# Kernel optimization log

Hardware: AMD Instinct MI355X
Metric: run time of the kernel (lower is better)

The kernel has to match this reference:

```python
import jax, jax.numpy as jnp
from jax import lax
import numpy as np

EPS = 1e-5
COMMITMENT = 0.25


def conv1d(x, w, b, pad):
    # x: [N,C,T], w: [O,I,K]
    y = lax.conv_general_dilated(x, w, window_strides=(1,), padding=[(pad, pad)],
                                 dimension_numbers=('NCH', 'OIH', 'NCH'))
    return y + b[None, :, None]


def batchnorm(x, g, b):
    # training-mode BN (PyTorch default): batch stats over (N, T), biased var
    m = jnp.mean(x, axis=(0, 2), keepdims=True)
    v = jnp.var(x, axis=(0, 2), keepdims=True)
    return (x - m) * lax.rsqrt(v + EPS) * g[None, :, None] + b[None, :, None]


def setup_inputs() -> dict:
    key = jax.random.key(0)
    ks = jax.random.split(key, 16)
    B, C_in, T = 16, 80, 4096
    H1, H2, D, K = 128, 256, 64, 512
    s = 0.05
    inp = {
        'x': jax.random.normal(ks[0], (B, C_in, T), jnp.float32),
        # encoder
        'enc_w1': jax.random.normal(ks[1], (H1, C_in, 3), jnp.float32) * s,
        'enc_b1': jnp.zeros((H1,), jnp.float32),
        'bn1_g': jnp.ones((H1,), jnp.float32), 'bn1_b': jnp.zeros((H1,), jnp.float32),
        'enc_w2': jax.random.normal(ks[2], (H2, H1, 3), jnp.float32) * s,
        'enc_b2': jnp.zeros((H2,), jnp.float32),
        'bn2_g': jnp.ones((H2,), jnp.float32), 'bn2_b': jnp.zeros((H2,), jnp.float32),
        'enc_w3': jax.random.normal(ks[3], (D, H2, 1), jnp.float32) * s,
        'enc_b3': jnp.zeros((D,), jnp.float32),
        # codebook, init uniform(-1/K, 1/K) like the torch module
        'codebook': jax.random.uniform(ks[4], (K, D), jnp.float32, -1.0 / K, 1.0 / K),
        # decoder (hidden_dims reversed: [256, 128])
        'dec_w1': jax.random.normal(ks[5], (H2, D, 3), jnp.float32) * s,
        'dec_b1': jnp.zeros((H2,), jnp.float32),
        'dbn1_g': jnp.ones((H2,), jnp.float32), 'dbn1_b': jnp.zeros((H2,), jnp.float32),
        'dec_w2': jax.random.normal(ks[6], (H1, H2, 3), jnp.float32) * s,
        'dec_b2': jnp.zeros((H1,), jnp.float32),
        'dbn2_g': jnp.ones((H1,), jnp.float32), 'dbn2_b': jnp.zeros((H1,), jnp.float32),
        'dec_w3': jax.random.normal(ks[7], (C_in, H1, 3), jnp.float32) * s,
        'dec_b3': jnp.zeros((C_in,), jnp.float32),
    }
    return inp


def _vqvae(x, enc_w1, enc_b1, bn1_g, bn1_b, enc_w2, enc_b2, bn2_g, bn2_b,
           enc_w3, enc_b3, codebook, dec_w1, dec_b1, dbn1_g, dbn1_b,
           dec_w2, dec_b2, dbn2_g, dbn2_b, dec_w3, dec_b3):
    # ---- Encoder ----
    h = jax.nn.relu(batchnorm(conv1d(x, enc_w1, enc_b1, 1), bn1_g, bn1_b))
    h = jax.nn.relu(batchnorm(conv1d(h, enc_w2, enc_b2, 1), bn2_g, bn2_b))
    z = conv1d(h, enc_w3, enc_b3, 0)  # [B, D, T]

    # ---- Vector Quantizer ----
    B, D, T = z.shape
    zt = jnp.transpose(z, (0, 2, 1))            # [B, T, D]
    flat = zt.reshape(-1, D)                    # [B*T, D]
    # squared L2 distances to codebook [B*T, K]
    d2 = (jnp.sum(flat * flat, axis=1, keepdims=True)
          + jnp.sum(codebook * codebook, axis=1)
          - 2.0 * flat @ codebook.T)
    idx = jnp.argmin(d2, axis=1)                # [B*T]
    quantized = codebook[idx].reshape(B, T, D)  # gather == onehot @ codebook

    e_latent_loss = jnp.mean((lax.stop_gradient(quantized) - zt) ** 2)
    q_latent_loss = jnp.mean((quantized - lax.stop_gradient(zt)) ** 2)
    vq_loss = q_latent_loss + COMMITMENT * e_latent_loss

    # straight-through estimator
    q_st = zt + lax.stop_gradient(quantized - zt)
    q_st = jnp.transpose(q_st, (0, 2, 1))       # [B, D, T]
    encoding_indices = idx.reshape(B, T)

    # ---- Decoder ----
    h = conv1d(q_st, dec_w1, dec_b1, 1)
    h = conv1d(jax.nn.relu(batchnorm(h, dbn1_g, dbn1_b)), dec_w2, dec_b2, 1)
    recon = conv1d(jax.nn.relu(batchnorm(h, dbn2_g, dbn2_b)), dec_w3, dec_b3, 1)
    return recon, vq_loss, encoding_indices


def reference(x, enc_w1, enc_b1, bn1_g, bn1_b, enc_w2, enc_b2, bn2_g, bn2_b,
              enc_w3, enc_b3, codebook, dec_w1, dec_b1, dbn1_g, dbn1_b,
              dec_w2, dec_b2, dbn2_g, dbn2_b, dec_w3, dec_b3):
    return _vqvae(x, enc_w1, enc_b1, bn1_g, bn1_b, enc_w2, enc_b2, bn2_g, bn2_b,
                  enc_w3, enc_b3, codebook, dec_w1, dec_b1, dbn1_g, dbn1_b,
                  dec_w2, dec_b2, dbn2_g, dbn2_b, dec_w3, dec_b3)
```

## Files before the change

### kernel.cpp

```cpp
#include <hip/hip_runtime.h>
#include <math.h>

#define N_B 16
#define T_LEN 4096

typedef float f32x4  __attribute__((ext_vector_type(4)));
typedef _Float16 half8 __attribute__((ext_vector_type(8)));

static const size_t OFF_A    = 0;
static const size_t OFF_B    = 8388608;
static const size_t OFF_Z    = 25165824;
static const size_t OFF_WS   = 29360128;
static const size_t OFF_CBS  = 29540352;
static const size_t OFF_C2   = 29683712;
static const size_t OFF_ST   = 29684736;
static const size_t OFF_LOSS = 29685760;

static const size_t WS_E1 = 0;
static const size_t WS_E2 = 36864;
static const size_t WS_E3 = 135168;
static const size_t WS_D1 = 0;
static const size_t WS_D2 = 49152;
static const size_t WS_D3 = 147456;

__device__ inline void f2h2(float v, short& hi, short& lo) {
    _Float16 h = (_Float16)v;
    float r = (v - (float)h) * 4096.0f;
    _Float16 l = (_Float16)r;
    hi = __builtin_bit_cast(short, h);
    lo = __builtin_bit_cast(short, l);
}

template<int C_IN, int C_OUT, int KS>
__device__ inline void wsplit_fill(const float* __restrict__ w,
                                   short* __restrict__ dst, int e) {
    int i  = e & 31;
    int r  = e >> 5;
    int co = r % C_OUT;
    int r2 = r / C_OUT;
    int k  = r2 % KS;
    int c  = r2 / KS;
    int ci = c * 32 + i;
    float v = (ci < C_IN) ? w[((size_t)co * C_IN + ci) * KS + k] : 0.f;
    short h, l; f2h2(v, h, l);
    size_t base = ((size_t)(c * KS + k) * 2 * C_OUT + co) * 32 + i;
    dst[base] = h;
    dst[base + (size_t)C_OUT * 32] = l;
}

__global__ __launch_bounds__(256) void prep_k(
        const float* __restrict__ w1, const float* __restrict__ w2,
        const float* __restrict__ w3, const float* __restrict__ cb,
        float* wsf) {
    int e = blockIdx.x * 256 + threadIdx.x;
    if (e < 36864)        wsplit_fill<80, 128, 3>(w1, (short*)(wsf + OFF_WS + WS_E1), e);
    else if (e < 135168)  wsplit_fill<128, 256, 3>(w2, (short*)(wsf + OFF_WS + WS_E2), e - 36864);
    else if (e < 151552)  wsplit_fill<256, 64, 1>(w3, (short*)(wsf + OFF_WS + WS_E3), e - 135168);
    else if (e < 152064) {
        int c = e - 151552;
        const float* p = cb + (size_t)c * 64;
        double s = 0.0;
        for (int d = 0; d < 64; ++d) { double v = p[d]; s += v * v; }
        wsf[OFF_C2 + c] = (float)s;
    } else if (e < 184832) {
        int e2   = e - 152064;
        int i    = e2 & 31;
        int r    = e2 >> 5;
        int code = r & 511;
        int ks   = r >> 9;
        float v  = cb[(size_t)code * 64 + ks * 32 + i];
        short h, l; f2h2(v, h, l);
        short* dst = (short*)(wsf + OFF_CBS);
        dst[((size_t)(ks * 2 + 0) * 512 + code) * 32 + i] = h;
        dst[((size_t)(ks * 2 + 1) * 512 + code) * 32 + i] = l;
    } else if (e == 184832) {
        *(double*)(wsf + OFF_LOSS) = 0.0;
    }
}

__global__ __launch_bounds__(256) void prep2_k(
        const float* __restrict__ wd1, const float* __restrict__ wd2,
        const float* __restrict__ wd3, float* wsf) {
    int e = blockIdx.x * 256 + threadIdx.x;
    if (e < 49152)        wsplit_fill<64, 256, 3>(wd1, (short*)(wsf + OFF_WS + WS_D1), e);
    else if (e < 147456)  wsplit_fill<256, 128, 3>(wd2, (short*)(wsf + OFF_WS + WS_D2), e - 49152);
    else if (e < 178176)  wsplit_fill<128, 80, 3>(wd3, (short*)(wsf + OFF_WS + WS_D3), e - 147456);
}

template<int C_IN, int C_OUT, int KS, bool BN_IN>
__global__ __launch_bounds__(256, 3) void fconv_k(
        const float* __restrict__ x, const short* __restrict__ wsp,
        const float* __restrict__ bias, const float2* __restrict__ stats,
        float* __restrict__ out) {
    constexpr int NCH  = (C_IN + 31) / 32;
    constexpr int HALO = KS / 2;
    constexpr int TT   = (KS == 1) ? 64 : 128;
    constexpr int NTT  = TT / 16;
    constexpr int NTILE = T_LEN / TT;
    constexpr int XR   = TT + KS - 1;
    constexpr int RS   = 72;
    constexpr int LO   = 40;
    constexpr int TQ   = TT / 4;

    __shared__ __align__(16) short xs[XR * RS];

    const int tid  = threadIdx.x;
    const int lane = tid & 63;
    const int wv   = tid >> 6;
    const int ln   = lane & 15;
    const int q    = lane >> 4;

    const int n    = blockIdx.x / NTILE;
    const int t0   = (blockIdx.x % NTILE) * TT;
    const int co0  = blockIdx.y * 64;
    const int co_l = co0 + wv * 16 + ln;

    f32x4 a0[NTT], a1[NTT];
#pragma unroll
    for (int tt = 0; tt < NTT; ++tt)
#pragma unroll
        for (int i = 0; i < 4; ++i) { a0[tt][i] = 0.f; a1[tt][i] = 0.f; }

#pragma unroll 1
    for (int c = 0; c < NCH; ++c) {
        half8 ah[KS], al[KS];
        {
            half8 z = {0, 0, 0, 0, 0, 0, 0, 0};
#pragma unroll
            for (int k = 0; k < KS; ++k) {
                const short* wp = wsp
                    + ((size_t)(c * KS + k) * 2 * C_OUT + co_l) * 32 + q * 8;
                ah[k] = (co_l < C_OUT) ? *(const half8*)wp : z;
                al[k] = (co_l < C_OUT) ? *(const half8*)(wp + (size_t)C_OUT * 32) : z;
            }
        }

        __syncthreads();
        for (int e = tid; e < 32 * TQ; e += 256) {
            const int ci  = e / TQ;
            const int tq  = e % TQ;
            const int cig = c * 32 + ci;
            float v[4] = {0.f, 0.f, 0.f, 0.f};
            if (cig < C_IN) {
                const float* xp = x + ((size_t)(n * C_IN + cig)) * T_LEN + t0 + tq;
#pragma unroll
                for (int j = 0; j < 4; ++j) v[j] = xp[TQ * j];
                if constexpr (BN_IN) {
                    float2 s = stats[cig];
#pragma unroll
                    for (int j = 0; j < 4; ++j) v[j] = fmaxf(fmaf(v[j], s.x, s.y), 0.f);
                }
            }
#pragma unroll
            for (int j = 0; j < 4; ++j) {
                short h, l; f2h2(v[j], h, l);
                short* p = &xs[(HALO + tq + TQ * j) * RS + ci];
                p[0]  = h;
                p[LO] = l;
            }
        }
        if constexpr (KS == 3) {
            if (tid < 64) {
                const int ci   = tid & 31;
                const int side = tid >> 5;
                const int cig  = c * 32 + ci;
                const int gt   = side ? (t0 + TT) : (t0 - 1);
                float v = 0.f;
                if (cig < C_IN && gt >= 0 && gt < T_LEN) {
                    v = x[((size_t)(n * C_IN + cig)) * T_LEN + gt];
                    if constexpr (BN_IN) {
                        float2 s = stats[cig];
                        v = fmaxf(fmaf(v, s.x, s.y), 0.f);
                    }
                }
                short h, l; f2h2(v, h, l);
                short* p = &xs[(side ? (XR - 1) : 0) * RS + ci];
                p[0] = h; p[LO] = l;
            }
        }
        __syncthreads();

#pragma unroll
        for (int k = 0; k < KS; ++k) {
#pragma unroll
            for (int tt = 0; tt < NTT; ++tt) {
                const short* xr = &xs[(tt * 16 + ln + k) * RS + q * 8];
                half8 bh = *(const half8*)&xr[0];
                half8 bl = *(const half8*)&xr[LO];
                a0[tt] = __builtin_amdgcn_mfma_f32_16x16x32_f16(ah[k], bh, a0[tt], 0, 0, 0);
                a1[tt] = __builtin_amdgcn_mfma_f32_16x16x32_f16(ah[k], bl, a1[tt], 0, 0, 0);
                a1[tt] = __builtin_amdgcn_mfma_f32_16x16x32_f16(al[k], bh, a1[tt], 0, 0, 0);
            }
        }
    }

#pragma unroll
    for (int r = 0; r < 4; ++r) {
        const int co = co0 + wv * 16 + q * 4 + r;
        if (co < C_OUT) {
            const float bv = bias[co];
            float* op = out + ((size_t)(n * C_OUT + co)) * T_LEN + t0 + ln;
#pragma unroll
            for (int tt = 0; tt < NTT; ++tt)
                op[tt * 16] = fmaf(a1[tt][r], 0.000244140625f, a0[tt][r]) + bv;
        }
    }
}

__global__ __launch_bounds__(256) void stats1_k(
        const float* __restrict__ y, int C, double2* __restrict__ part) {
    int c = blockIdx.x % C, n = blockIdx.x / C;
    int tid = threadIdx.x;
    const float* p = y + ((size_t)(n * C + c)) * T_LEN;
    double s1 = 0.0, s2 = 0.0;
    for (int t = tid; t < T_LEN; t += 256) {
        double v = p[t];
        s1 += v; s2 += v * v;
    }
    __shared__ double r1[256], r2[256];
    r1[tid] = s1; r2[tid] = s2;
    __syncthreads();
    for (int s = 128; s > 0; s >>= 1) {
        if (tid < s) { r1[tid] += r1[tid + s]; r2[tid] += r2[tid + s]; }
        __syncthreads();
    }
    if (tid == 0) part[(size_t)c * N_B + n] = make_double2(r1[0], r2[0]);
}

__global__ __launch_bounds__(256) void stats2_k(
        const double2* __restrict__ part, int C, const float* __restrict__ g,
        const float* __restrict__ b, float2* __restrict__ stats) {
    int c = blockIdx.x * 256 + threadIdx.x;
    if (c >= C) return;
    double s1 = 0.0, s2 = 0.0;
    for (int n = 0; n < N_B; ++n) {
        double2 v = part[(size_t)c * N_B + n];
        s1 += v.x; s2 += v.y;
    }
    double m   = s1 / 65536.0;
    double var = s2 / 65536.0 - m * m;
    double sc  = (double)g[c] / sqrt(var + 1e-5);
    stats[c] = make_float2((float)sc, (float)((double)b[c] - m * sc));
}

__global__ __launch_bounds__(256) void vq_k(
        const float* __restrict__ z, const float* __restrict__ cb,
        const short* __restrict__ cbs, const float* __restrict__ c2,
        float* __restrict__ q, float* __restrict__ idx_out,
        double* __restrict__ loss) {
    __shared__ __align__(16) float zs[64 * 68];
    __shared__ __align__(16) short zh[64 * 136];
    __shared__ float  c2s[512];
    __shared__ float  szf_s[64];
    __shared__ int    idxs[64];
    __shared__ double dred[256];

    const int tid  = threadIdx.x;
    const int lane = tid & 63;
    const int wv   = tid >> 6;
    const int ln   = lane & 15;
    const int q4   = lane >> 4;
    const int n    = blockIdx.x >> 6;
    const int t0   = (blockIdx.x & 63) * 64;

    for (int e = tid; e < 512; e += 256) c2s[e] = c2[e];
    for (int e = tid; e < 1024; e += 256) {
        const int d  = e >> 4;
        const int tq = e & 15;
        const float* zp = z + ((size_t)(n * 64 + d)) * T_LEN + t0 + tq;
        const int ks = d >> 5, i = d & 31;
#pragma unroll
        for (int j = 0; j < 4; ++j) {
            const int t = tq + 16 * j;
            float v = zp[16 * j];
            zs[t * 68 + d] = v;
            short h, l; f2h2(v, h, l);
            zh[t * 136 + (ks * 2 + 0) * 32 + i] = h;
            zh[t * 136 + (ks * 2 + 1) * 32 + i] = l;
        }
    }
    __syncthreads();
    if (tid < 64) {
        double s = 0.0;
        const float* zr = &zs[tid * 68];
        for (int d = 0; d < 64; ++d) { double v = zr[d]; s += v * v; }
        szf_s[tid] = (float)s;
    }
    __syncthreads();

    const short* zr = &zh[(wv * 16 + ln) * 136 + q4 * 8];
    const half8 bh0 = *(const half8*)&zr[0];
    const half8 bl0 = *(const half8*)&zr[32];
    const half8 bh1 = *(const half8*)&zr[64];
    const half8 bl1 = *(const half8*)&zr[96];
    const float As  = szf_s[wv * 16 + ln];

    float bs = 3.0e38f;
    int   bi = 1 << 30;

#pragma unroll 4
    for (int ct = 0; ct < 32; ++ct) {
        const short* ap = cbs + ((size_t)(ct * 16 + ln)) * 32 + q4 * 8;
        const half8 ah0 = *(const half8*)&ap[0];
        const half8 al0 = *(const half8*)&ap[512 * 32];
        const half8 ah1 = *(const half8*)&ap[2 * 512 * 32];
        const half8 al1 = *(const half8*)&ap[3 * 512 * 32];
        f32x4 a0 = {0.f, 0.f, 0.f, 0.f};
        f32x4 a1 = {0.f, 0.f, 0.f, 0.f};
        a0 = __builtin_amdgcn_mfma_f32_16x16x32_f16(ah0, bh0, a0, 0, 0, 0);
        a1 = __builtin_amdgcn_mfma_f32_16x16x32_f16(ah0, bl0, a1, 0, 0, 0);
        a1 = __builtin_amdgcn_mfma_f32_16x16x32_f16(al0, bh0, a1, 0, 0, 0);
        a0 = __builtin_amdgcn_mfma_f32_16x16x32_f16(ah1, bh1, a0, 0, 0, 0);
        a1 = __builtin_amdgcn_mfma_f32_16x16x32_f16(ah1, bl1, a1, 0, 0, 0);
        a1 = __builtin_amdgcn_mfma_f32_16x16x32_f16(al1, bh1, a1, 0, 0, 0);
#pragma unroll
        for (int r = 0; r < 4; ++r) {
            const int code = ct * 16 + q4 * 4 + r;
            const float m32 = fmaf(a1[r], 0.000244140625f, a0[r]);
            const float A   = As + c2s[code];
            const float s   = A - 2.0f * m32;
            if (s < bs || (s == bs && code < bi)) { bs = s; bi = code; }
        }
    }
#pragma unroll
    for (int off = 16; off <= 32; off <<= 1) {
        const float os = __shfl_xor(bs, off);
        const int   oi = __shfl_xor(bi, off);
        if (os < bs || (os == bs && oi < bi)) { bs = os; bi = oi; }
    }
    if (q4 == 0) {
        const int t = wv * 16 + ln;
        idxs[t] = bi;
        idx_out[(size_t)n * T_LEN + t0 + t] = (float)bi;
    }
    __syncthreads();

    {
        const int g = tid >> 6, t = tid & 63;
        const int bi2 = idxs[t];
        double ls = 0.0;
        for (int dd = 0; dd < 16; ++dd) {
            const int d = g * 16 + dd;
            const float qv = cb[(size_t)bi2 * 64 + d];
            const float zv = zs[t * 68 + d];
            const double df = (double)qv - (double)zv;
            ls += df * df;
            q[((size_t)(n * 64 + d)) * T_LEN + t0 + t] = qv;
        }
        dred[tid] = ls;
    }
    __syncthreads();
    for (int s = 128; s > 0; s >>= 1) {
        if (tid < s) dred[tid] += dred[tid + s];
        __syncthreads();
    }
    if (tid == 0) atomicAdd(loss, dred[0]);
}

__global__ void fin_k(const double* __restrict__ loss, float* __restrict__ out) {
    if (threadIdx.x == 0 && blockIdx.x == 0)
        out[0] = (float)(1.25 * (*loss) / 4194304.0);
}

extern "C" void kernel_launch(void* const* d_in, const int* in_sizes, int n_in,
                              void* d_out, int out_size, void* d_ws, size_t ws_size,
                              hipStream_t stream) {
    const float* x      = (const float*)d_in[0];
    const float* enc_w1 = (const float*)d_in[1];
    const float* enc_b1 = (const float*)d_in[2];
    const float* bn1_g  = (const float*)d_in[3];
    const float* bn1_b  = (const float*)d_in[4];
    const float* enc_w2 = (const float*)d_in[5];
    const float* enc_b2 = (const float*)d_in[6];
    const float* bn2_g  = (const float*)d_in[7];
    const float* bn2_b  = (const float*)d_in[8];
    const float* enc_w3 = (const float*)d_in[9];
    const float* enc_b3 = (const float*)d_in[10];
    const float* cb     = (const float*)d_in[11];
    const float* dec_w1 = (const float*)d_in[12];
    const float* dec_b1 = (const float*)d_in[13];
    const float* dbn1_g = (const float*)d_in[14];
    const float* dbn1_b = (const float*)d_in[15];
    const float* dec_w2 = (const float*)d_in[16];
    const float* dec_b2 = (const float*)d_in[17];
    const float* dbn2_g = (const float*)d_in[18];
    const float* dbn2_b = (const float*)d_in[19];
    const float* dec_w3 = (const float*)d_in[20];
    const float* dec_b3 = (const float*)d_in[21];

    float* wsf   = (float*)d_ws;
    float* outf  = (float*)d_out;
    float* A     = wsf + OFF_A;
    float* Bb    = wsf + OFF_B;
    float* Z     = wsf + OFF_Z;
    float2* st   = (float2*)(wsf + OFF_ST);
    double* lossp = (double*)(wsf + OFF_LOSS);
    double2* partA = (double2*)A;
    double2* partB = (double2*)Bb;

    const short* wsE1 = (const short*)(wsf + OFF_WS + WS_E1);
    const short* wsE2 = (const short*)(wsf + OFF_WS + WS_E2);
    const short* wsE3 = (const short*)(wsf + OFF_WS + WS_E3);
    const short* wsD1 = (const short*)(wsf + OFF_WS + WS_D1);
    const short* wsD2 = (const short*)(wsf + OFF_WS + WS_D2);
    const short* wsD3 = (const short*)(wsf + OFF_WS + WS_D3);
    const short* cbs  = (const short*)(wsf + OFF_CBS);

    prep_k<<<723, 256, 0, stream>>>(enc_w1, enc_w2, enc_w3, cb, wsf);

    fconv_k<80, 128, 3, false><<<dim3(512, 2), 256, 0, stream>>>(
        x, wsE1, enc_b1, nullptr, A);
    stats1_k<<<128 * N_B, 256, 0, stream>>>(A, 128, partB);
    stats2_k<<<1, 256, 0, stream>>>(partB, 128, bn1_g, bn1_b, st);
    fconv_k<128, 256, 3, true><<<dim3(512, 4), 256, 0, stream>>>(
        A, wsE2, enc_b2, st, Bb);
    stats1_k<<<256 * N_B, 256, 0, stream>>>(Bb, 256, partA);
    stats2_k<<<1, 256, 0, stream>>>(partA, 256, bn2_g, bn2_b, st);
    fconv_k<256, 64, 1, true><<<dim3(1024, 1), 256, 0, stream>>>(
        Bb, wsE3, enc_b3, st, Z);

    prep2_k<<<696, 256, 0, stream>>>(dec_w1, dec_w2, dec_w3, wsf);

    vq_k<<<1024, 256, 0, stream>>>(Z, cb, cbs, wsf + OFF_C2, Z,
                                   outf + 5242881, lossp);
    fin_k<<<1, 64, 0, stream>>>(lossp, outf + 5242880);

    fconv_k<64, 256, 3, false><<<dim3(512, 4), 256, 0, stream>>>(
        Z, wsD1, dec_b1, nullptr, Bb);
    stats1_k<<<256 * N_B, 256, 0, stream>>>(Bb, 256, partA);
    stats2_k<<<1, 256, 0, stream>>>(partA, 256, dbn1_g, dbn1_b, st);
    fconv_k<256, 128, 3, true><<<dim3(512, 2), 256, 0, stream>>>(
        Bb, wsD2, dec_b2, st, A);
    stats1_k<<<128 * N_B, 256, 0, stream>>>(A, 128, partB);
    stats2_k<<<1, 256, 0, stream>>>(partB, 128, dbn2_g, dbn2_b, st);
    fconv_k<128, 80, 3, true><<<dim3(512, 2), 256, 0, stream>>>(
        A, wsD3, dec_b3, st, outf);
}
```

Before: 412.4 us.

## Switch convs to 32x32 MFMA tiles and fuse BN stats into conv epilogue

The conv kernel moves from 16x16x32 MFMA to 32x32x16 MFMA with a 2x2 wave layout and separate hi/lo LDS planes, and the split weights are repacked in 16-channel groups. Each conv epilogue now produces per-block double sums and sum-of-squares, so the separate stats1/stats2 passes that re-read the full activation are replaced by a single small reduction kernel. A runtime self-test of the MFMA layout is added with a scalar FMA fallback path. The occupancy hint drops from 3 to 2 blocks per SM to accommodate the larger accumulators.

Measured after the change: 553.4 us. 34.2% more time.

```diff
diff --git a/kernel.cpp b/kernel.cpp
--- a/kernel.cpp
+++ b/kernel.cpp
@@ -5,7 +5,10 @@
 #define T_LEN 4096
 
 typedef float f32x4  __attribute__((ext_vector_type(4)));
+typedef float f32x16 __attribute__((ext_vector_type(16)));
 typedef _Float16 half8 __attribute__((ext_vector_type(8)));
+
+struct LL { long a, b; };
 
 static const size_t OFF_A    = 0;
 static const size_t OFF_B    = 8388608;
@@ -30,22 +33,25 @@
     hi = __builtin_bit_cast(short, h);
     lo = __builtin_bit_cast(short, l);
 }
+__device__ inline float h2f(short s) {
+    return (float)__builtin_bit_cast(_Float16, s);
+}
 
 template<int C_IN, int C_OUT, int KS>
 __device__ inline void wsplit_fill(const float* __restrict__ w,
                                    short* __restrict__ dst, int e) {
-    int i  = e & 31;
-    int r  = e >> 5;
+    int i  = e & 15;
+    int r  = e >> 4;
     int co = r % C_OUT;
     int r2 = r / C_OUT;
     int k  = r2 % KS;
-    int c  = r2 / KS;
-    int ci = c * 32 + i;
+    int c2 = r2 / KS;
+    int ci = c2 * 16 + i;
     float v = (ci < C_IN) ? w[((size_t)co * C_IN + ci) * KS + k] : 0.f;
     short h, l; f2h2(v, h, l);
-    size_t base = ((size_t)(c * KS + k) * 2 * C_OUT + co) * 32 + i;
+    size_t base = ((size_t)(c2 * KS + k) * 2 * C_OUT + co) * 16 + i;
     dst[base] = h;
-    dst[base + (size_t)C_OUT * 32] = l;
+    dst[base + (size_t)C_OUT * 16] = l;
 }
 
 __global__ __launch_bounds__(256) void prep_k(
@@ -87,54 +93,72 @@
     else if (e < 178176)  wsplit_fill<128, 80, 3>(wd3, (short*)(wsf + OFF_WS + WS_D3), e - 147456);
 }
 
-template<int C_IN, int C_OUT, int KS, bool BN_IN>
-__global__ __launch_bounds__(256, 3) void fconv_k(
+template<int C_IN, int C_OUT, int KS, bool BN_IN, bool STATS>
+__global__ __launch_bounds__(256, 2) void fconv_k(
         const float* __restrict__ x, const short* __restrict__ wsp,
         const float* __restrict__ bias, const float2* __restrict__ stats,
-        float* __restrict__ out) {
-    constexpr int NCH  = (C_IN + 31) / 32;
-    constexpr int HALO = KS / 2;
-    constexpr int TT   = (KS == 1) ? 64 : 128;
-    constexpr int NTT  = TT / 16;
+        float* __restrict__ out, double2* __restrict__ part) {
+    constexpr int NCH   = (C_IN + 31) / 32;
+    constexpr int HALO  = KS / 2;
+    constexpr int TT    = (KS == 1) ? 64 : 128;
+    constexpr int HT    = TT / 2;
+    constexpr int NTT   = HT / 32;
     constexpr int NTILE = T_LEN / TT;
-    constexpr int XR   = TT + KS - 1;
-    constexpr int RS   = 72;
-    constexpr int LO   = 40;
-    constexpr int TQ   = TT / 4;
-
-    __shared__ __align__(16) short xs[XR * RS];
+    constexpr int XR    = TT + KS - 1;
+    constexpr int RS2   = 36;
+    constexpr int TQ    = TT / 4;
+
+    __shared__ __align__(16) short xh[XR * RS2];
+    __shared__ __align__(16) short xl[XR * RS2];
+    __shared__ int okf;
 
     const int tid  = threadIdx.x;
     const int lane = tid & 63;
     const int wv   = tid >> 6;
-    const int ln   = lane & 15;
-    const int q    = lane >> 4;
+    const int wr   = wv >> 1;
+    const int wc   = wv & 1;
+    const int nn   = lane & 31;
+    const int hsel = lane >> 5;
 
     const int n    = blockIdx.x / NTILE;
     const int t0   = (blockIdx.x % NTILE) * TT;
     const int co0  = blockIdx.y * 64;
-    const int co_l = co0 + wv * 16 + ln;
-
-    f32x4 a0[NTT], a1[NTT];
+    const int co_l = co0 + wr * 32 + nn;
+
+    bool ok = true;
+    {
+        half8 pa, pb;
+#pragma unroll
+        for (int j = 0; j < 8; ++j) {
+            int k = hsel * 8 + j;
+            pa[j] = (_Float16)(float)(nn + 2 * k);
+            pb[j] = (_Float16)(float)(nn + 3 * k);
+        }
+        f32x16 pd;
+#pragma unroll
+        for (int r = 0; r < 16; ++r) pd[r] = 0.f;
+        pd = __builtin_amdgcn_mfma_f32_32x32x16_f16(pa, pb, pd, 0, 0, 0);
+#pragma unroll
+        for (int r = 0; r < 16; ++r) {
+            int m = (r & 3) + 8 * (r >> 2) + 4 * hsel;
+            float e = (float)(16 * m * nn + 360 * m + 240 * nn + 7440);
+            if (pd[r] != e) ok = false;
+        }
+    }
+    if (tid == 0) okf = 1;
+    __syncthreads();
+    if (!ok) okf = 0;
+    __syncthreads();
+    const bool okp = (okf != 0);
+
+    f32x16 a0[NTT], a1[NTT];
 #pragma unroll
     for (int tt = 0; tt < NTT; ++tt)
 #pragma unroll
-        for (int i = 0; i < 4; ++i) { a0[tt][i] = 0.f; a1[tt][i] = 0.f; }
+        for (int r = 0; r < 16; ++r) { a0[tt][r] = 0.f; a1[tt][r] = 0.f; }
 
 #pragma unroll 1
     for (int c = 0; c < NCH; ++c) {
-        half8 ah[KS], al[KS];
-        {
-            half8 z = {0, 0, 0, 0, 0, 0, 0, 0};
-#pragma unroll
-            for (int k = 0; k < KS; ++k) {
-                const short* wp = wsp
-                    + ((size_t)(c * KS + k) * 2 * C_OUT + co_l) * 32 + q * 8;
-                ah[k] = (co_l < C_OUT) ? *(const half8*)wp : z;
-                al[k] = (co_l < C_OUT) ? *(const half8*)(wp + (size_t)C_OUT * 32) : z;
-            }
-        }
-
         __syncthreads();
         for (int e = tid; e < 32 * TQ; e += 256) {
             const int ci  = e / TQ;
@@ -145,77 +169,147 @@
                 const float* xp = x + ((size_t)(n * C_IN + cig)) * T_LEN + t0 + tq;
 #pragma unroll
                 for (int j = 0; j < 4; ++j) v[j] = xp[TQ * j];
-                if constexpr (BN_IN) {
-                    float2 s = stats[cig];
-#pragma unroll
-                    for (int j = 0; j < 4; ++j) v[j] = fmaxf(fmaf(v[j], s.x, s.y), 0.f);
+                if (BN_IN) {
+                    float2 sst = stats[cig];
+#pragma unroll
+                    for (int j = 0; j < 4; ++j) v[j] = fmaxf(fmaf(v[j], sst.x, sst.y), 0.f);
                 }
             }
 #pragma unroll
             for (int j = 0; j < 4; ++j) {
                 short h, l; f2h2(v[j], h, l);
-                short* p = &xs[(HALO + tq + TQ * j) * RS + ci];
-                p[0]  = h;
-                p[LO] = l;
+                const int row = HALO + tq + TQ * j;
+                xh[row * RS2 + ci] = h;
+                xl[row * RS2 + ci] = l;
             }
         }
-        if constexpr (KS == 3) {
+        if (KS == 3) {
             if (tid < 64) {
                 const int ci   = tid & 31;
                 const int side = tid >> 5;
                 const int cig  = c * 32 + ci;
                 const int gt   = side ? (t0 + TT) : (t0 - 1);
-                float v = 0.f;
+                float vv = 0.f;
                 if (cig < C_IN && gt >= 0 && gt < T_LEN) {
-                    v = x[((size_t)(n * C_IN + cig)) * T_LEN + gt];
-                    if constexpr (BN_IN) {
-                        float2 s = stats[cig];
-                        v = fmaxf(fmaf(v, s.x, s.y), 0.f);
+                    vv = x[((size_t)(n * C_IN + cig)) * T_LEN + gt];
+                    if (BN_IN) {
+                        float2 sst = stats[cig];
+                        vv = fmaxf(fmaf(vv, sst.x, sst.y), 0.f);
                     }
                 }
-                short h, l; f2h2(v, h, l);
-                short* p = &xs[(side ? (XR - 1) : 0) * RS + ci];
-                p[0] = h; p[LO] = l;
+                short h, l; f2h2(vv, h, l);
+                const int row = side ? (XR - 1) : 0;
+                xh[row * RS2 + ci] = h;
+                xl[row * RS2 + ci] = l;
             }
         }
         __syncthreads();
 
-#pragma unroll
-        for (int k = 0; k < KS; ++k) {
-#pragma unroll
-            for (int tt = 0; tt < NTT; ++tt) {
-                const short* xr = &xs[(tt * 16 + ln + k) * RS + q * 8];
-                half8 bh = *(const half8*)&xr[0];
-                half8 bl = *(const half8*)&xr[LO];
-                a0[tt] = __builtin_amdgcn_mfma_f32_16x16x32_f16(ah[k], bh, a0[tt], 0, 0, 0);
-                a1[tt] = __builtin_amdgcn_mfma_f32_16x16x32_f16(ah[k], bl, a1[tt], 0, 0, 0);
-                a1[tt] = __builtin_amdgcn_mfma_f32_16x16x32_f16(al[k], bh, a1[tt], 0, 0, 0);
+        if (okp) {
+#pragma unroll
+            for (int s = 0; s < 2; ++s) {
+                const int c2 = c * 2 + s;
+                half8 ah[KS], al[KS];
+                half8 z8 = {0, 0, 0, 0, 0, 0, 0, 0};
+#pragma unroll
+                for (int k = 0; k < KS; ++k) {
+                    const short* wp = wsp
+                        + ((size_t)(c2 * KS + k) * 2 * C_OUT + co_l) * 16 + hsel * 8;
+                    ah[k] = (co_l < C_OUT) ? *(const half8*)wp : z8;
+                    al[k] = (co_l < C_OUT) ? *(const half8*)(wp + (size_t)C_OUT * 16) : z8;
+                }
+#pragma unroll
+                for (int k = 0; k < KS; ++k) {
+#pragma unroll
+                    for (int tt = 0; tt < NTT; ++tt) {
+                        const int row = wc * HT + tt * 32 + nn + k;
+                        const int col = s * 16 + hsel * 8;
+                        const short* ph = &xh[row * RS2 + col];
+                        const short* pl = &xl[row * RS2 + col];
+                        LL th, tl;
+                        th.a = *(const long*)ph; th.b = *(const long*)(ph + 4);
+                        tl.a = *(const long*)pl; tl.b = *(const long*)(pl + 4);
+                        half8 bh = __builtin_bit_cast(half8, th);
+                        half8 bl = __builtin_bit_cast(half8, tl);
+                        a0[tt] = __builtin_amdgcn_mfma_f32_32x32x16_f16(ah[k], bh, a0[tt], 0, 0, 0);
+                        a1[tt] = __builtin_amdgcn_mfma_f32_32x32x16_f16(ah[k], bl, a1[tt], 0, 0, 0);
+                        a1[tt] = __builtin_amdgcn_mfma_f32_32x32x16_f16(al[k], bh, a1[tt], 0, 0, 0);
+                    }
+                }
             }
-        }
-    }
-
-#pragma unroll
-    for (int r = 0; r < 4; ++r) {
-        const int co = co0 + wv * 16 + q * 4 + r;
-        if (co < C_OUT) {
-            const float bv = bias[co];
-            float* op = out + ((size_t)(n * C_OUT + co)) * T_LEN + t0 + ln;
-#pragma unroll
-            for (int tt = 0; tt < NTT; ++tt)
-                op[tt * 16] = fmaf(a1[tt][r], 0.000244140625f, a0[tt][r]) + bv;
-        }
-    }
-}
-
-__global__ __launch_bounds__(256) void stats1_k(
-        const float* __restrict__ y, int C, double2* __restrict__ part) {
-    int c = blockIdx.x % C, n = blockIdx.x / C;
-    int tid = threadIdx.x;
-    const float* p = y + ((size_t)(n * C + c)) * T_LEN;
+        } else {
+#pragma unroll 1
+            for (int s = 0; s < 2; ++s) {
+                const int c2 = c * 2 + s;
+#pragma unroll 1
+                for (int k = 0; k < KS; ++k) {
+#pragma unroll 1
+                    for (int i = 0; i < 16; ++i) {
+                        float wvv[16];
+#pragma unroll
+                        for (int r = 0; r < 16; ++r) {
+                            const int m  = (r & 3) + 8 * (r >> 2) + 4 * hsel;
+                            const int co = co0 + wr * 32 + m;
+                            float vv = 0.f;
+                            if (co < C_OUT) {
+                                const size_t bb =
+                                    ((size_t)(c2 * KS + k) * 2 * C_OUT + co) * 16 + i;
+                                vv = h2f(wsp[bb])
+                                   + h2f(wsp[bb + (size_t)C_OUT * 16]) * 0.000244140625f;
+                            }
+                            wvv[r] = vv;
+                        }
+#pragma unroll
+                        for (int tt = 0; tt < NTT; ++tt) {
+                            const int row = wc * HT + tt * 32 + nn + k;
+                            const int col = s * 16 + i;
+                            const float xv = h2f(xh[row * RS2 + col])
+                                           + h2f(xl[row * RS2 + col]) * 0.000244140625f;
+#pragma unroll
+                            for (int r = 0; r < 16; ++r)
+                                a0[tt][r] = fmaf(wvv[r], xv, a0[tt][r]);
+                        }
+                    }
+                }
+            }
+        }
+    }
+
+    const int plinear = (blockIdx.y * gridDim.x + blockIdx.x) * 2 + wc;
+#pragma unroll
+    for (int r = 0; r < 16; ++r) {
+        const int m  = (r & 3) + 8 * (r >> 2) + 4 * hsel;
+        const int co = co0 + wr * 32 + m;
+        const float bv = (co < C_OUT) ? bias[co] : 0.f;
+        double s1 = 0.0, s2 = 0.0;
+#pragma unroll
+        for (int tt = 0; tt < NTT; ++tt) {
+            const float v = fmaf(a1[tt][r], 0.000244140625f, a0[tt][r]) + bv;
+            if (co < C_OUT)
+                out[((size_t)(n * C_OUT + co)) * T_LEN + t0 + wc * HT + tt * 32 + nn] = v;
+            if (STATS) { s1 += (double)v; s2 += (double)v * (double)v; }
+        }
+        if (STATS) {
+#pragma unroll
+            for (int off = 1; off <= 16; off <<= 1) {
+                s1 += __shfl_xor(s1, off);
+                s2 += __shfl_xor(s2, off);
+            }
+            if (nn == 0)
+                part[(size_t)plinear * 64 + wr * 32 + m] = make_double2(s1, s2);
+        }
+    }
+}
+
+__global__ __launch_bounds__(256) void stats_k(
+        const double2* __restrict__ part, const float* __restrict__ g,
+        const float* __restrict__ b, float2* __restrict__ stats) {
+    const int c = blockIdx.x;
+    const int tid = threadIdx.x;
     double s1 = 0.0, s2 = 0.0;
-    for (int t = tid; t < T_LEN; t += 256) {
-        double v = p[t];
-        s1 += v; s2 += v * v;
+    for (int j = tid; j < 1024; j += 256) {
+        double2 v = part[((size_t)(c >> 6) * 1024 + j) * 64 + (c & 63)];
+        s1 += v.x; s2 += v.y;
     }
     __shared__ double r1[256], r2[256];
     r1[tid] = s1; r2[tid] = s2;
@@ -224,23 +318,12 @@
         if (tid < s) { r1[tid] += r1[tid + s]; r2[tid] += r2[tid + s]; }
         __syncthreads();
     }
-    if (tid == 0) part[(size_t)c * N_B + n] = make_double2(r1[0], r2[0]);
-}
-
-__global__ __launch_bounds__(256) void stats2_k(
-        const double2* __restrict__ part, int C, const float* __restrict__ g,
-        const float* __restrict__ b, float2* __restrict__ stats) {
-    int c = blockIdx.x * 256 + threadIdx.x;
-    if (c >= C) return;
-    double s1 = 0.0, s2 = 0.0;
-    for (int n = 0; n < N_B; ++n) {
-        double2 v = part[(size_t)c * N_B + n];
-        s1 += v.x; s2 += v.y;
-    }
-    double m   = s1 / 65536.0;
-    double var = s2 / 65536.0 - m * m;
-    double sc  = (double)g[c] / sqrt(var + 1e-5);
-    stats[c] = make_float2((float)sc, (float)((double)b[c] - m * sc));
+    if (tid == 0) {
+        double m   = r1[0] / 65536.0;
+        double var = r2[0] / 65536.0 - m * m;
+        double sc  = (double)g[c] / sqrt(var + 1e-5);
+        stats[c] = make_float2((float)sc, (float)((double)b[c] - m * sc));
+    }
 }
 
 __global__ __launch_bounds__(256) void vq_k(
@@ -395,8 +478,6 @@
     float* Z     = wsf + OFF_Z;
     float2* st   = (float2*)(wsf + OFF_ST);
     double* lossp = (double*)(wsf + OFF_LOSS);
-    double2* partA = (double2*)A;
-    double2* partB = (double2*)Bb;
 
     const short* wsE1 = (const short*)(wsf + OFF_WS + WS_E1);
     const short* wsE2 = (const short*)(wsf + OFF_WS + WS_E2);
@@ -406,18 +487,21 @@
     const short* wsD3 = (const short*)(wsf + OFF_WS + WS_D3);
     const short* cbs  = (const short*)(wsf + OFF_CBS);
 
+    double2* pE1 = (double2*)Bb;
+    double2* pE2 = (double2*)Z;
+    double2* pD1 = (double2*)A;
+    double2* pD2 = (double2*)Z;
+
     prep_k<<<723, 256, 0, stream>>>(enc_w1, enc_w2, enc_w3, cb, wsf);
 
-    fconv_k<80, 128, 3, false><<<dim3(512, 2), 256, 0, stream>>>(
-        x, wsE1, enc_b1, nullptr, A);
-    stats1_k<<<128 * N_B, 256, 0, stream>>>(A, 128, partB);
-    stats2_k<<<1, 256, 0, stream>>>(partB, 128, bn1_g, bn1_b, st);
-    fconv_k<128, 256, 3, true><<<dim3(512, 4), 256, 0, stream>>>(
-        A, wsE2, enc_b2, st, Bb);
-    stats1_k<<<256 * N_B, 256, 0, stream>>>(Bb, 256, partA);
-    stats2_k<<<1, 256, 0, stream>>>(partA, 256, bn2_g, bn2_b, st);
-    fconv_k<256, 64, 1, true><<<dim3(1024, 1), 256, 0, stream>>>(
-        Bb, wsE3, enc_b3, st, Z);
+    fconv_k<80, 128, 3, false, true><<<dim3(512, 2), 256, 0, stream>>>(
+        x, wsE1, enc_b1, nullptr, A, pE1);
+    stats_k<<<128, 256, 0, stream>>>(pE1, bn1_g, bn1_b, st);
+    fconv_k<128, 256, 3, true, true><<<dim3(512, 4), 256, 0, stream>>>(
+        A, wsE2, enc_b2, st, Bb, pE2);
+    stats_k<<<256, 256, 0, stream>>>(pE2, bn2_g, bn2_b, st);
+    fconv_k<256, 64, 1, true, false><<<dim3(1024, 1), 256, 0, stream>>>(
+        Bb, wsE3, enc_b3, st, Z, nullptr);
 
     prep2_k<<<696, 256, 0, stream>>>(dec_w1, dec_w2, dec_w3, wsf);
 
@@ -425,14 +509,12 @@
                                    outf + 5242881, lossp);
     fin_k<<<1, 64, 0, stream>>>(lossp, outf + 5242880);
 
-    fconv_k<64, 256, 3, false><<<dim3(512, 4), 256, 0, stream>>>(
-        Z, wsD1, dec_b1, nullptr, Bb);
-    stats1_k<<<256 * N_B, 256, 0, stream>>>(Bb, 256, partA);
-    stats2_k<<<1, 256, 0, stream>>>(partA, 256, dbn1_g, dbn1_b, st);
-    fconv_k<256, 128, 3, true><<<dim3(512, 2), 256, 0, stream>>>(
-        Bb, wsD2, dec_b2, st, A);
-    stats1_k<<<128 * N_B, 256, 0, stream>>>(A, 128, partB);
-    stats2_k<<<1, 256, 0, stream>>>(partB, 128, dbn2_g, dbn2_b, st);
-    fconv_k<128, 80, 3, true><<<dim3(512, 2), 256, 0, stream>>>(
-        A, wsD3, dec_b3, st, outf);
-}
+    fconv_k<64, 256, 3, false, true><<<dim3(512, 4), 256, 0, stream>>>(
+        Z, wsD1, dec_b1, nullptr, Bb, pD1);
+    stats_k<<<256, 256, 0, stream>>>(pD1, dbn1_g, dbn1_b, st);
+    fconv_k<256, 128, 3, true, true><<<dim3(512, 2), 256, 0, stream>>>(
+        Bb, wsD2, dec_b2, st, A, pD2);
+    stats_k<<<128, 256, 0, stream>>>(pD2, dbn2_g, dbn2_b, st);
+    fconv_k<128, 80, 3, true, false><<<dim3(512, 2), 256, 0, stream>>>(
+        A, wsD3, dec_b3, st, outf, nullptr);
+}
```

## Fuse BatchNorm statistics partial sums into conv epilogue

Applied to the files above, without the earlier changes.

The conv kernel epilogue now accumulates per-channel sum and sum of squares over its tile, reduces them with lane shuffles, and writes float2 partials per block. The separate stats pass, which re-read each full activation tensor from memory, is replaced by a small kernel that reduces those partials in double precision. This removes four full-tensor reads and two launches per BN layer pair. The trade-off is float32 accumulation within a tile instead of double, and partial buffers that alias other workspace regions.

Measured after the change: 380.3 us. -7.8%, faster.

```diff
diff --git a/kernel.cpp b/kernel.cpp
--- a/kernel.cpp
+++ b/kernel.cpp
@@ -29,6 +29,9 @@
     _Float16 l = (_Float16)r;
     hi = __builtin_bit_cast(short, h);
     lo = __builtin_bit_cast(short, l);
+}
+__device__ inline float h2f(short s) {
+    return (float)__builtin_bit_cast(_Float16, s);
 }
 
 template<int C_IN, int C_OUT, int KS>
@@ -87,11 +90,11 @@
     else if (e < 178176)  wsplit_fill<128, 80, 3>(wd3, (short*)(wsf + OFF_WS + WS_D3), e - 147456);
 }
 
-template<int C_IN, int C_OUT, int KS, bool BN_IN>
+template<int C_IN, int C_OUT, int KS, bool BN_IN, bool STATS>
 __global__ __launch_bounds__(256, 3) void fconv_k(
         const float* __restrict__ x, const short* __restrict__ wsp,
         const float* __restrict__ bias, const float2* __restrict__ stats,
-        float* __restrict__ out) {
+        float* __restrict__ out, float2* __restrict__ part) {
     constexpr int NCH  = (C_IN + 31) / 32;
     constexpr int HALO = KS / 2;
     constexpr int TT   = (KS == 1) ? 64 : 128;
@@ -145,7 +148,7 @@
                 const float* xp = x + ((size_t)(n * C_IN + cig)) * T_LEN + t0 + tq;
 #pragma unroll
                 for (int j = 0; j < 4; ++j) v[j] = xp[TQ * j];
-                if constexpr (BN_IN) {
+                if (BN_IN) {
                     float2 s = stats[cig];
 #pragma unroll
                     for (int j = 0; j < 4; ++j) v[j] = fmaxf(fmaf(v[j], s.x, s.y), 0.f);
@@ -159,7 +162,7 @@
                 p[LO] = l;
             }
         }
-        if constexpr (KS == 3) {
+        if (KS == 3) {
             if (tid < 64) {
                 const int ci   = tid & 31;
                 const int side = tid >> 5;
@@ -168,7 +171,7 @@
                 float v = 0.f;
                 if (cig < C_IN && gt >= 0 && gt < T_LEN) {
                     v = x[((size_t)(n * C_IN + cig)) * T_LEN + gt];
-                    if constexpr (BN_IN) {
+                    if (BN_IN) {
                         float2 s = stats[cig];
                         v = fmaxf(fmaf(v, s.x, s.y), 0.f);
                     }
@@ -194,28 +197,43 @@
         }
     }
 
+    const int plinear = blockIdx.y * (N_B * NTILE) + blockIdx.x;
 #pragma unroll
     for (int r = 0; r < 4; ++r) {
         const int co = co0 + wv * 16 + q * 4 + r;
+        float s1 = 0.f, s2 = 0.f;
         if (co < C_OUT) {
             const float bv = bias[co];
             float* op = out + ((size_t)(n * C_OUT + co)) * T_LEN + t0 + ln;
 #pragma unroll
-            for (int tt = 0; tt < NTT; ++tt)
-                op[tt * 16] = fmaf(a1[tt][r], 0.000244140625f, a0[tt][r]) + bv;
-        }
-    }
-}
-
-__global__ __launch_bounds__(256) void stats1_k(
-        const float* __restrict__ y, int C, double2* __restrict__ part) {
-    int c = blockIdx.x % C, n = blockIdx.x / C;
-    int tid = threadIdx.x;
-    const float* p = y + ((size_t)(n * C + c)) * T_LEN;
+            for (int tt = 0; tt < NTT; ++tt) {
+                const float v = fmaf(a1[tt][r], 0.000244140625f, a0[tt][r]) + bv;
+                op[tt * 16] = v;
+                if (STATS) { s1 += v; s2 = fmaf(v, v, s2); }
+            }
+        }
+        if (STATS) {
+#pragma unroll
+            for (int off = 1; off <= 8; off <<= 1) {
+                s1 += __shfl_xor(s1, off);
+                s2 += __shfl_xor(s2, off);
+            }
+            if (ln == 0)
+                part[(size_t)plinear * 64 + wv * 16 + q * 4 + r] =
+                    make_float2(s1, s2);
+        }
+    }
+}
+
+__global__ __launch_bounds__(256) void stats_k(
+        const float2* __restrict__ part, const float* __restrict__ g,
+        const float* __restrict__ b, float2* __restrict__ stats) {
+    const int c = blockIdx.x;
+    const int tid = threadIdx.x;
     double s1 = 0.0, s2 = 0.0;
-    for (int t = tid; t < T_LEN; t += 256) {
-        double v = p[t];
-        s1 += v; s2 += v * v;
+    for (int j = tid; j < 512; j += 256) {
+        float2 v = part[((size_t)(c >> 6) * 512 + j) * 64 + (c & 63)];
+        s1 += (double)v.x; s2 += (double)v.y;
     }
     __shared__ double r1[256], r2[256];
     r1[tid] = s1; r2[tid] = s2;
@@ -224,23 +242,12 @@
         if (tid < s) { r1[tid] += r1[tid + s]; r2[tid] += r2[tid + s]; }
         __syncthreads();
     }
-    if (tid == 0) part[(size_t)c * N_B + n] = make_double2(r1[0], r2[0]);
-}
-
-__global__ __launch_bounds__(256) void stats2_k(
-        const double2* __restrict__ part, int C, const float* __restrict__ g,
-        const float* __restrict__ b, float2* __restrict__ stats) {
-    int c = blockIdx.x * 256 + threadIdx.x;
-    if (c >= C) return;
-    double s1 = 0.0, s2 = 0.0;
-    for (int n = 0; n < N_B; ++n) {
-        double2 v = part[(size_t)c * N_B + n];
-        s1 += v.x; s2 += v.y;
-    }
-    double m   = s1 / 65536.0;
-    double var = s2 / 65536.0 - m * m;
-    double sc  = (double)g[c] / sqrt(var + 1e-5);
-    stats[c] = make_float2((float)sc, (float)((double)b[c] - m * sc));
+    if (tid == 0) {
+        double m   = r1[0] / 65536.0;
+        double var = r2[0] / 65536.0 - m * m;
+        double sc  = (double)g[c] / sqrt(var + 1e-5);
+        stats[c] = make_float2((float)sc, (float)((double)b[c] - m * sc));
+    }
 }
 
 __global__ __launch_bounds__(256) void vq_k(
@@ -395,8 +402,6 @@
     float* Z     = wsf + OFF_Z;
     float2* st   = (float2*)(wsf + OFF_ST);
     double* lossp = (double*)(wsf + OFF_LOSS);
-    double2* partA = (double2*)A;
-    double2* partB = (double2*)Bb;
 
     const short* wsE1 = (const short*)(wsf + OFF_WS + WS_E1);
     const short* wsE2 = (const short*)(wsf + OFF_WS + WS_E2);
@@ -406,18 +411,21 @@
     const short* wsD3 = (const short*)(wsf + OFF_WS + WS_D3);
     const short* cbs  = (const short*)(wsf + OFF_CBS);
 
+    float2* pE1 = (float2*)Bb;
+    float2* pE2 = (float2*)Z;
+    float2* pD1 = (float2*)A;
+    float2* pD2 = (float2*)Z;
+
     prep_k<<<723, 256, 0, stream>>>(enc_w1, enc_w2, enc_w3, cb, wsf);
 
-    fconv_k<80, 128, 3, false><<<dim3(512, 2), 256, 0, stream>>>(
-        x, wsE1, enc_b1, nullptr, A);
-    stats1_k<<<128 * N_B, 256, 0, stream>>>(A, 128, partB);
-    stats2_k<<<1, 256, 0, stream>>>(partB, 128, bn1_g, bn1_b, st);
-    fconv_k<128, 256, 3, true><<<dim3(512, 4), 256, 0, stream>>>(
-        A, wsE2, enc_b2, st, Bb);
-    stats1_k<<<256 * N_B, 256, 0, stream>>>(Bb, 256, partA);
-    stats2_k<<<1, 256, 0, stream>>>(partA, 256, bn2_g, bn2_b, st);
-    fconv_k<256, 64, 1, true><<<dim3(1024, 1), 256, 0, stream>>>(
-        Bb, wsE3, enc_b3, st, Z);
+    fconv_k<80, 128, 3, false, true><<<dim3(512, 2), 256, 0, stream>>>(
+        x, wsE1, enc_b1, nullptr, A, pE1);
+    stats_k<<<128, 256, 0, stream>>>(pE1, bn1_g, bn1_b, st);
+    fconv_k<128, 256, 3, true, true><<<dim3(512, 4), 256, 0, stream>>>(
+        A, wsE2, enc_b2, st, Bb, pE2);
+    stats_k<<<256, 256, 0, stream>>>(pE2, bn2_g, bn2_b, st);
+    fconv_k<256, 64, 1, true, false><<<dim3(1024, 1), 256, 0, stream>>>(
+        Bb, wsE3, enc_b3, st, Z, nullptr);
 
     prep2_k<<<696, 256, 0, stream>>>(dec_w1, dec_w2, dec_w3, wsf);
 
@@ -425,14 +433,12 @@
                                    outf + 5242881, lossp);
     fin_k<<<1, 64, 0, stream>>>(lossp, outf + 5242880);
 
-    fconv_k<64, 256, 3, false><<<dim3(512, 4), 256, 0, stream>>>(
-        Z, wsD1, dec_b1, nullptr, Bb);
-    stats1_k<<<256 * N_B, 256, 0, stream>>>(Bb, 256, partA);
-    stats2_k<<<1, 256, 0, stream>>>(partA, 256, dbn1_g, dbn1_b, st);
-    fconv_k<256, 128, 3, true><<<dim3(512, 2), 256, 0, stream>>>(
-        Bb, wsD2, dec_b2, st, A);
-    stats1_k<<<128 * N_B, 256, 0, stream>>>(A, 128, partB);
-    stats2_k<<<1, 256, 0, stream>>>(partB, 128, dbn2_g, dbn2_b, st);
-    fconv_k<128, 80, 3, true><<<dim3(512, 2), 256, 0, stream>>>(
-        A, wsD3, dec_b3, st, outf);
-}
+    fconv_k<64, 256, 3, false, true><<<dim3(512, 4), 256, 0, stream>>>(
+        Z, wsD1, dec_b1, nullptr, Bb, pD1);
+    stats_k<<<256, 256, 0, stream>>>(pD1, dbn1_g, dbn1_b, st);
+    fconv_k<256, 128, 3, true, true><<<dim3(512, 2), 256, 0, stream>>>(
+        Bb, wsD2, dec_b2, st, A, pD2);
+    stats_k<<<128, 256, 0, stream>>>(pD2, dbn2_g, dbn2_b, st);
+    fconv_k<128, 80, 3, true, false><<<dim3(512, 2), 256, 0, stream>>>(
+        A, wsD3, dec_b3, st, outf, nullptr);
+}
```
